# Performance work log

Measured on AMD Instinct MI355X. Metric: run time of the kernel, lower is better.

## Reference

```python
import jax, jax.numpy as jnp
import numpy as np

DIM = 384
HEADS = 6
HEAD_DIM = 64
WIN = 14
SCALE = HEAD_DIM ** -0.5
EPS = 1e-5  # torch LayerNorm default


def setup_inputs() -> dict:
    key = jax.random.key(0)
    ks = jax.random.split(key, 8)
    w = lambda k, shape: jax.random.normal(k, shape, dtype=jnp.float32) * 0.02
    return {
        "x": jax.random.normal(ks[0], (1, 336, 336, DIM), dtype=jnp.float32),
        "qkv_w": w(ks[1], (DIM, 3 * DIM)),
        "qkv_b": jnp.zeros((3 * DIM,), jnp.float32),
        "proj_w": w(ks[2], (DIM, DIM)),
        "proj_b": jnp.zeros((DIM,), jnp.float32),
        "rel_pos_h": w(ks[3], (2 * WIN - 1, HEAD_DIM)),
        "rel_pos_w": w(ks[4], (2 * WIN - 1, HEAD_DIM)),
        "norm1_w": jnp.ones((DIM,), jnp.float32),
        "norm1_b": jnp.zeros((DIM,), jnp.float32),
        "norm2_w": jnp.ones((DIM,), jnp.float32),
        "norm2_b": jnp.zeros((DIM,), jnp.float32),
        "fc1_w": w(ks[5], (DIM, 4 * DIM)),
        "fc1_b": jnp.zeros((4 * DIM,), jnp.float32),
        "fc2_w": w(ks[6], (4 * DIM, DIM)),
        "fc2_b": jnp.zeros((DIM,), jnp.float32),
    }


def _layernorm(x, w, b):
    m = jnp.mean(x, axis=-1, keepdims=True)
    v = jnp.var(x, axis=-1, keepdims=True)
    return (x - m) / jnp.sqrt(v + EPS) * w + b


def _rel_table(rel_pos):
    coords = np.arange(WIN)[:, None] - np.arange(WIN)[None, :] + (WIN - 1)
    return rel_pos[coords]


def _block(x, qkv_w, qkv_b, proj_w, proj_b, rel_pos_h, rel_pos_w,
           norm1_w, norm1_b, norm2_w, norm2_b, fc1_w, fc1_b, fc2_w, fc2_b):
    B, H, W, C = x.shape
    shortcut = x
    x = _layernorm(x, norm1_w, norm1_b)

    nH, nW = H // WIN, W // WIN
    xw = x.reshape(B, nH, WIN, nW, WIN, C).transpose(0, 1, 3, 2, 4, 5)
    xw = xw.reshape(B * nH * nW, WIN * WIN, C)  # [Nw, 196, C]
    Nw, L = xw.shape[0], WIN * WIN

    # --- attention with decomposed rel-pos ---
    qkv = xw @ qkv_w + qkv_b                         # [Nw, 196, 3C]
    qkv = qkv.reshape(Nw, L, 3, HEADS, HEAD_DIM).transpose(2, 0, 3, 1, 4)
    q, k, v = qkv[0], qkv[1], qkv[2]                 # [Nw, h, 196, d]

    attn = jnp.einsum("bhqd,bhkd->bhqk", q * SCALE, k)  # [Nw, h, 196, 196]

    Rh = _rel_table(rel_pos_h)                       # [14, 14, d]
    Rw = _rel_table(rel_pos_w)
    r_q = q.reshape(Nw, HEADS, WIN, WIN, HEAD_DIM)
    rel_h = jnp.einsum("bnhwc,hkc->bnhwk", r_q, Rh)  # [Nw, h, 14, 14, 14]
    rel_w = jnp.einsum("bnhwc,wkc->bnhwk", r_q, Rw)
    attn = (attn.reshape(Nw, HEADS, WIN, WIN, WIN, WIN)
            + rel_h[..., :, None] + rel_w[..., None, :]).reshape(Nw, HEADS, L, L)

    attn = jax.nn.softmax(attn, axis=-1)
    out = jnp.einsum("bhqk,bhkd->bhqd", attn, v)     # [Nw, h, 196, d]
    out = out.transpose(0, 2, 1, 3).reshape(Nw, L, C)
    out = out @ proj_w + proj_b

    # --- window unpartition ---
    out = out.reshape(B, nH, nW, WIN, WIN, C).transpose(0, 1, 3, 2, 4, 5)
    out = out.reshape(B, H, W, C)

    x = shortcut + out
    h = _layernorm(x, norm2_w, norm2_b)
    h = jax.nn.gelu(h @ fc1_w + fc1_b, approximate=False) @ fc2_w + fc2_b
    return x + h


def reference(x, qkv_w, qkv_b, proj_w, proj_b, rel_pos_h, rel_pos_w,
              norm1_w, norm1_b, norm2_w, norm2_b, fc1_w, fc1_b, fc2_w, fc2_b):
    return _block(x, qkv_w, qkv_b, proj_w, proj_b, rel_pos_h, rel_pos_w,
                  norm1_w, norm1_b, norm2_w, norm2_b, fc1_w, fc1_b, fc2_w, fc2_b)
```

## Files before the change

kernel.cpp:

```cpp
#include <hip/hip_runtime.h>
#include <math.h>

#define TOKENS 112896
#define C      384
#define NQKV   1152
#define NFC    1536
#define HEADS  6
#define HD     64
#define WIN    14
#define L      196
#define NWS    24
#define SCALEF 0.125f

typedef unsigned int  u32;
typedef unsigned short u16;
typedef short short8 __attribute__((ext_vector_type(8)));
typedef float floatx4 __attribute__((ext_vector_type(4)));

__device__ __forceinline__ u16 f2bf(float f) {
  u32 u = __float_as_uint(f);
  u += 0x7FFFu + ((u >> 16) & 1u);
  return (u16)(u >> 16);
}

__device__ __forceinline__ float bf2f(u16 v) {
  return __uint_as_float((u32)v << 16);
}

__device__ __forceinline__ u32 pk2bf(float lo, float hi) {
  u32 r;
  asm("v_cvt_pk_bf16_f32 %0, %1, %2" : "=v"(r) : "v"(lo), "v"(hi));
  return r;
}

__device__ __forceinline__ float gelu_f(float v) {
  float z = fabsf(v) * 0.70710678118654752f;
  float t = 1.0f / (1.0f + 0.3275911f * z);
  float poly = t * (0.254829592f + t * (-0.284496736f + t * (1.421413741f +
               t * (-1.453152027f + t * 1.061405429f))));
  float erfv = 1.0f - poly * __expf(-z * z);
  erfv = copysignf(erfv, v);
  return 0.5f * v * (1.0f + erfv);
}

__device__ __forceinline__ void async16(u16* lds, const u16* g) {
  __builtin_amdgcn_global_load_lds((const __attribute__((address_space(1))) void*)g,
                                   (__attribute__((address_space(3))) void*)lds,
                                   16, 0, 0);
}

__device__ __forceinline__ int win_to_tok(int r) {
  int n = r / L, l = r % L;
  int wh = n / NWS, ww = n % NWS;
  int ih = l / WIN, iw = l % WIN;
  return (wh * WIN + ih) * 336 + ww * WIN + iw;
}

__global__ __launch_bounds__(256) void conv_t_kernel(const float* __restrict__ in,
    u16* __restrict__ out, int K, int N)
{
  __shared__ u16 tile[32][33];
  const int kb = blockIdx.y * 32, nb = blockIdx.x * 32;
  const int tx = threadIdx.x & 31, ty = threadIdx.x >> 5;
#pragma unroll
  for (int i = 0; i < 4; i++) {
    int k = kb + ty + i * 8;
    tile[ty + i * 8][tx] = f2bf(in[(size_t)k * N + nb + tx]);
  }
  __syncthreads();
#pragma unroll
  for (int i = 0; i < 4; i++) {
    int n = nb + ty + i * 8;
    out[(size_t)n * K + kb + tx] = tile[tx][ty + i * 8];
  }
}

template<bool PERMUTE>
__global__ __launch_bounds__(128) void ln_kernel(const float* __restrict__ x,
    const float* __restrict__ w, const float* __restrict__ b,
    u16* __restrict__ out)
{
  const int t = blockIdx.x;
  const int tid = threadIdx.x;
  const float* xr = x + (size_t)t * C;
  float v0 = xr[tid], v1 = xr[tid + 128], v2 = xr[tid + 256];
  float s  = v0 + v1 + v2;
  float ss = v0 * v0 + v1 * v1 + v2 * v2;
#pragma unroll
  for (int off = 32; off > 0; off >>= 1) {
    s  += __shfl_down(s, off);
    ss += __shfl_down(ss, off);
  }
  __shared__ float red[4];
  if ((tid & 63) == 0) { red[(tid >> 6) * 2 + 0] = s; red[(tid >> 6) * 2 + 1] = ss; }
  __syncthreads();
  float S  = red[0] + red[2];
  float SS = red[1] + red[3];
  float mean = S * (1.0f / C);
  float var  = SS * (1.0f / C) - mean * mean;
  float rstd = rsqrtf(var + 1e-5f);
  size_t orow;
  if (PERMUTE) {
    int h_ = t / 336, w_ = t % 336;
    int wh = h_ / WIN, ih = h_ % WIN;
    int ww = w_ / WIN, iw = w_ % WIN;
    orow = (size_t)((wh * NWS + ww) * L + ih * WIN + iw);
  } else {
    orow = (size_t)t;
  }
  u16* op = out + orow * C;
  op[tid]       = f2bf((v0 - mean) * rstd * w[tid]       + b[tid]);
  op[tid + 128] = f2bf((v1 - mean) * rstd * w[tid + 128] + b[tid + 128]);
  op[tid + 256] = f2bf((v2 - mean) * rstd * w[tid + 256] + b[tid + 256]);
}

template<int MODE>
__global__ __launch_bounds__(256, 4) void gemm_bf16(
    const u16* __restrict__ A, const u16* __restrict__ Bt,
    const float* __restrict__ bias, const float* __restrict__ res,
    void* __restrict__ outv, int N, int K)
{
  __shared__ u16 As[2][128 * 32];
  __shared__ u16 Bs[2][128 * 32];
  const int tid = threadIdx.x;
  const int w = tid >> 6, l = tid & 63;

  const int nwg = gridDim.x * gridDim.y;
  int lin = blockIdx.y * gridDim.x + blockIdx.x;
  {
    int q8 = nwg >> 3, r8 = nwg & 7;
    int xcd = lin & 7, sub = lin >> 3;
    lin = (xcd < r8 ? xcd * (q8 + 1) : r8 * (q8 + 1) + (xcd - r8) * q8) + sub;
  }
  const int bx = lin % gridDim.x, by = lin / gridDim.x;
  const int bm = by * 128, bn = bx * 128;

  const int wm = (w >> 1) * 64, wn = (w & 1) * 64;
  const int lm = l & 15, quad = l >> 4;

  floatx4 acc[4][4] = {};

  u32 aofs[2], bofs[2];
#pragma unroll
  for (int q = 0; q < 2; q++) {
    int t = q * 256 + tid;
    int r = t >> 2, gl = t & 3;
    int sg = gl ^ ((r >> 1) & 3);
    aofs[q] = (u32)((bm + r) * K + sg * 8);
    bofs[q] = (u32)((bn + r) * K + sg * 8);
  }
  u16* Ad[2]; u16* Bd[2];
#pragma unroll
  for (int q = 0; q < 2; q++) {
    Ad[q] = &As[0][(q * 256 + w * 64) * 8];
    Bd[q] = &Bs[0][(q * 256 + w * 64) * 8];
  }

#define STAGE(buf, kt)                                         \
  {                                                            \
    const u16* Ap = A  + (kt);                                 \
    const u16* Bp = Bt + (kt);                                 \
    _Pragma("unroll")                                          \
    for (int q = 0; q < 2; q++) {                              \
      async16(Ad[q] + (buf) * 4096, Ap + aofs[q]);             \
      async16(Bd[q] + (buf) * 4096, Bp + bofs[q]);             \
    }                                                          \
  }

  const int xg = (quad ^ ((lm >> 1) & 3)) * 8;
  const u16* ard[4]; const u16* brd[4];
#pragma unroll
  for (int i = 0; i < 4; i++) {
    ard[i] = &As[0][(wm + i * 16 + lm) * 32 + xg];
    brd[i] = &Bs[0][(wn + i * 16 + lm) * 32 + xg];
  }

#define COMPUTE(BO)                                                         \
  {                                                                         \
    short8 bfr[4];                                                          \
    _Pragma("unroll")                                                       \
    for (int i2 = 0; i2 < 4; i2++)                                          \
      bfr[i2] = *(const short8*)(brd[i2] + (BO));                           \
    _Pragma("unroll")                                                       \
    for (int j2 = 0; j2 < 4; j2++) {                                        \
      short8 afr = *(const short8*)(ard[j2] + (BO));                        \
      _Pragma("unroll")                                                     \
      for (int i2 = 0; i2 < 4; i2++)                                        \
        acc[i2][j2] = __builtin_amdgcn_mfma_f32_16x16x32_bf16(              \
            bfr[i2], afr, acc[i2][j2], 0, 0, 0);                            \
    }                                                                       \
  }

  const int nk = K >> 5;
  STAGE(0, 0);
  __syncthreads();

  for (int t = 0; t < nk; t += 2) {
    STAGE(1, (t + 1) << 5);
    COMPUTE(0);
    __syncthreads();
    if (t + 2 < nk) STAGE(0, (t + 2) << 5);
    COMPUTE(4096);
    __syncthreads();
  }
#undef STAGE
#undef COMPUTE

  float4 bb[4];
#pragma unroll
  for (int i = 0; i < 4; i++)
    bb[i] = *(const float4*)&bias[bn + wn + i * 16 + quad * 4];

#pragma unroll
  for (int j = 0; j < 4; j++) {
    int m = bm + wm + j * 16 + lm;
    size_t ro;
    if (MODE == 1) ro = (size_t)win_to_tok(m) * N;
    else           ro = (size_t)m * N;
#pragma unroll
    for (int i = 0; i < 4; i++) {
      int n0 = bn + wn + i * 16 + quad * 4;
      float v0 = acc[i][j][0] + bb[i].x;
      float v1 = acc[i][j][1] + bb[i].y;
      float v2 = acc[i][j][2] + bb[i].z;
      float v3 = acc[i][j][3] + bb[i].w;
      if (MODE == 0) {
        uint2 st = make_uint2(pk2bf(v0, v1), pk2bf(v2, v3));
        *(uint2*)((u16*)outv + ro + n0) = st;
      } else if (MODE == 2) {
        uint2 st = make_uint2(pk2bf(gelu_f(v0), gelu_f(v1)),
                              pk2bf(gelu_f(v2), gelu_f(v3)));
        *(uint2*)((u16*)outv + ro + n0) = st;
      } else {
        float4 r4 = *(const float4*)&res[ro + n0];
        float4 o = make_float4(v0 + r4.x, v1 + r4.y, v2 + r4.z, v3 + r4.w);
        *(float4*)&((float*)outv)[ro + n0] = o;
      }
    }
  }
}

__global__ __launch_bounds__(256, 2) void attn_kernel(
    const u16* __restrict__ qkv,
    const float* __restrict__ relh, const float* __restrict__ relw,
    u16* __restrict__ out)
{
  __shared__ float Plds[4][512];
  __shared__ u16 rhlds[208 * 28];
  __shared__ u16 rwlds[208 * 28];
  __shared__ u16 Klds[32 * 64];
  __shared__ u16 Vtl[64 * 40];

  const int n = blockIdx.x / HEADS;
  const int h = blockIdx.x % HEADS;
  const int tid = threadIdx.x;
  const int w = tid >> 6;
  const int l = tid & 63;
  const int lm = l & 15;
  const int quad = l >> 4;
  const size_t base = (size_t)n * L;

  short8 qf[4][2];
#pragma unroll
  for (int i = 0; i < 4; i++) {
    int rt = w + 4 * i;
    if (rt <= 12) {
      int row = rt * 16 + lm; if (row > 195) row = 195;
      const u16* qp = qkv + (base + row) * NQKV + h * HD + quad * 8;
#pragma unroll
      for (int kf = 0; kf < 2; kf++)
        qf[i][kf] = *(const short8*)(qp + kf * 32);
    }
  }

  {
    short8 tf[2][2][2];
#pragma unroll
    for (int tab = 0; tab < 2; tab++) {
      const float* tp = tab ? relw : relh;
#pragma unroll
      for (int ct = 0; ct < 2; ct++) {
        int t = ct * 16 + lm;
#pragma unroll
        for (int kf = 0; kf < 2; kf++) {
          short8 v = {0, 0, 0, 0, 0, 0, 0, 0};
          if (t < 27) {
            const float* p = tp + t * HD + kf * 32 + quad * 8;
            float4 a = *(const float4*)p;
            float4 b = *(const float4*)(p + 4);
            v[0] = (short)f2bf(a.x); v[1] = (short)f2bf(a.y);
            v[2] = (short)f2bf(a.z); v[3] = (short)f2bf(a.w);
            v[4] = (short)f2bf(b.x); v[5] = (short)f2bf(b.y);
            v[6] = (short)f2bf(b.z); v[7] = (short)f2bf(b.w);
          }
          tf[tab][ct][kf] = v;
        }
      }
    }
#pragma unroll
    for (int i = 0; i < 4; i++) {
      int rt = w + 4 * i;
      if (rt > 12) continue;
#pragma unroll
      for (int tab = 0; tab < 2; tab++) {
        u16* dst = tab ? rwlds : rhlds;
#pragma unroll
        for (int ct = 0; ct < 2; ct++) {
          floatx4 acc = {};
          acc = __builtin_amdgcn_mfma_f32_16x16x32_bf16(qf[i][0], tf[tab][ct][0], acc, 0, 0, 0);
          acc = __builtin_amdgcn_mfma_f32_16x16x32_bf16(qf[i][1], tf[tab][ct][1], acc, 0, 0, 0);
          int t = ct * 16 + lm;
          if (t < 28) {
#pragma unroll
            for (int reg = 0; reg < 4; reg++) {
              int q = rt * 16 + quad * 4 + reg;
              dst[q * 28 + t] = f2bf(acc[reg]);
            }
          }
        }
      }
    }
  }

  floatx4 oacc[4][4] = {};
  float lsum[4][4] = {};

#pragma unroll 1
  for (int ks = 0; ks < 7; ks++) {
    __syncthreads();
    {
      int r = tid >> 3, g = tid & 7;
      int row = ks * 32 + r; if (row > 195) row = 195;
      uint4 kd = *(const uint4*)(qkv + (base + row) * NQKV + C + h * HD + g * 8);
      *(uint4*)&Klds[r * 64 + ((g ^ (r & 7)) * 8)] = kd;
    }
    {
      int r = tid & 31, seg = tid >> 5;
      int row = ks * 32 + r; if (row > 195) row = 195;
      uint4 vd = *(const uint4*)(qkv + (base + row) * NQKV + 2 * C + h * HD + seg * 8);
      union { uint4 u; u16 s[8]; } vv; vv.u = vd;
#pragma unroll
      for (int j = 0; j < 8; j++) Vtl[(seg * 8 + j) * 40 + r] = vv.s[j];
    }
    __syncthreads();

    short8 kfr[2][2];
#pragma unroll
    for (int ct = 0; ct < 2; ct++) {
      int krow = ct * 16 + lm;
#pragma unroll
      for (int kf = 0; kf < 2; kf++)
        kfr[ct][kf] = *(const short8*)&Klds[krow * 64 + (((kf * 4 + quad) ^ (krow & 7)) * 8)];
    }
    short8 vfr[4];
#pragma unroll
    for (int dt = 0; dt < 4; dt++)
      vfr[dt] = *(const short8*)&Vtl[(dt * 16 + lm) * 40 + quad * 8];

#pragma unroll
    for (int i = 0; i < 4; i++) {
      int rt = w + 4 * i;
      if (rt > 12) continue;
      floatx4 sc[2] = {};
#pragma unroll
      for (int ct = 0; ct < 2; ct++) {
        sc[ct] = __builtin_amdgcn_mfma_f32_16x16x32_bf16(qf[i][0], kfr[ct][0], sc[ct], 0, 0, 0);
        sc[ct] = __builtin_amdgcn_mfma_f32_16x16x32_bf16(qf[i][1], kfr[ct][1], sc[ct], 0, 0, 0);
      }
      float* Pw = Plds[w];
#pragma unroll
      for (int ct = 0; ct < 2; ct++) {
        int k = ks * 32 + ct * 16 + lm;
        int kh = (k * 293) >> 12;
        int kw2 = k - kh * 14;
        bool kval = (k < 196);
#pragma unroll
        for (int reg = 0; reg < 4; reg++) {
          int q = rt * 16 + quad * 4 + reg;
          int qh = (q * 293) >> 12;
          int qw = q - qh * 14;
          int th = qh - kh + 13; th = th < 0 ? 0 : th;
          int tw = qw - kw2 + 13;
          float bh = bf2f(rhlds[q * 28 + th]);
          float bw = bf2f(rwlds[q * 28 + tw]);
          float s = sc[ct][reg] * SCALEF + bh + bw;
          float p = kval ? __expf(s) : 0.0f;
          lsum[i][reg] += p;
          int prow = quad * 4 + reg;
          int col = ct * 16 + lm;
          Pw[prow * 32 + (((col >> 2) ^ (prow & 7)) * 4) + (col & 3)] = p;
        }
      }
      floatx4 pa = *(const floatx4*)&Pw[lm * 32 + (((2 * quad) ^ (lm & 7)) * 4)];
      floatx4 pb = *(const floatx4*)&Pw[lm * 32 + (((2 * quad + 1) ^ (lm & 7)) * 4)];
      short8 pfr;
#pragma unroll
      for (int j = 0; j < 4; j++) {
        pfr[j]     = (short)f2bf(pa[j]);
        pfr[4 + j] = (short)f2bf(pb[j]);
      }
#pragma unroll
      for (int dt = 0; dt < 4; dt++)
        oacc[i][dt] = __builtin_amdgcn_mfma_f32_16x16x32_bf16(pfr, vfr[dt], oacc[i][dt], 0, 0, 0);
    }
  }

#pragma unroll
  for (int i = 0; i < 4; i++) {
    int rt = w + 4 * i;
    if (rt > 12) continue;
#pragma unroll
    for (int reg = 0; reg < 4; reg++) {
      float v = lsum[i][reg];
      v += __shfl_xor(v, 1);
      v += __shfl_xor(v, 2);
      v += __shfl_xor(v, 4);
      v += __shfl_xor(v, 8);
      float inv = 1.0f / v;
      int row = rt * 16 + quad * 4 + reg;
      if (row < 196) {
        u16* op = out + (base + row) * C + h * HD + lm;
#pragma unroll
        for (int dt = 0; dt < 4; dt++) op[dt * 16] = f2bf(oacc[i][dt][reg] * inv);
      }
    }
  }
}

extern "C" void kernel_launch(void* const* d_in, const int* in_sizes, int n_in,
                              void* d_out, int out_size, void* d_ws, size_t ws_size,
                              hipStream_t stream)
{
  const float* x      = (const float*)d_in[0];
  const float* qkv_w  = (const float*)d_in[1];
  const float* qkv_b  = (const float*)d_in[2];
  const float* proj_w = (const float*)d_in[3];
  const float* proj_b = (const float*)d_in[4];
  const float* rel_h  = (const float*)d_in[5];
  const float* rel_w  = (const float*)d_in[6];
  const float* n1w    = (const float*)d_in[7];
  const float* n1b    = (const float*)d_in[8];
  const float* n2w    = (const float*)d_in[9];
  const float* n2b    = (const float*)d_in[10];
  const float* fc1_w  = (const float*)d_in[11];
  const float* fc1_b  = (const float*)d_in[12];
  const float* fc2_w  = (const float*)d_in[13];
  const float* fc2_b  = (const float*)d_in[14];

  u16*  W0 = (u16*)d_ws;
  u16*  W1 = (u16*)((char*)d_ws + 86704128);
  float* W2 = (float*)((char*)d_ws + 86704128 + 346816512);
  u16*  WT = (u16*)((char*)d_ws + 86704128 + 346816512 + 173408256);
  u16* qkv_wT  = WT;
  u16* proj_wT = qkv_wT + 442368;
  u16* fc1_wT  = proj_wT + 147456;
  u16* fc2_wT  = fc1_wT + 589824;

  conv_t_kernel<<<dim3(NQKV / 32, C / 32), 256, 0, stream>>>(qkv_w, qkv_wT, C, NQKV);
  conv_t_kernel<<<dim3(C / 32, C / 32), 256, 0, stream>>>(proj_w, proj_wT, C, C);
  conv_t_kernel<<<dim3(NFC / 32, C / 32), 256, 0, stream>>>(fc1_w, fc1_wT, C, NFC);
  conv_t_kernel<<<dim3(C / 32, NFC / 32), 256, 0, stream>>>(fc2_w, fc2_wT, NFC, C);

  ln_kernel<true><<<TOKENS, 128, 0, stream>>>(x, n1w, n1b, W0);
  gemm_bf16<0><<<dim3(NQKV / 128, TOKENS / 128), 256, 0, stream>>>(
      W0, qkv_wT, qkv_b, nullptr, W1, NQKV, C);
  attn_kernel<<<576 * HEADS, 256, 0, stream>>>(W1, rel_h, rel_w, W0);
  gemm_bf16<1><<<dim3(C / 128, TOKENS / 128), 256, 0, stream>>>(
      W0, proj_wT, proj_b, x, W2, C, C);
  ln_kernel<false><<<TOKENS, 128, 0, stream>>>(W2, n2w, n2b, W0);
  gemm_bf16<2><<<dim3(NFC / 128, TOKENS / 128), 256, 0, stream>>>(
      W0, fc1_wT, fc1_b, nullptr, W1, NFC, C);
  gemm_bf16<3><<<dim3(C / 128, TOKENS / 128), 256, 0, stream>>>(
      W1, fc2_wT, fc2_b, W2, (float*)d_out, C, NFC);
}
```

Measured before the change: 1.415 ms.

## Load GEMM MFMA fragments directly from global memory into registers, dropping LDS staging

Replaces the LDS double-buffered async global-to-LDS staging in the bf16 GEMM with direct per-lane global loads of MFMA fragments into registers, double-buffered in registers. This removes the LDS traffic and the __syncthreads barriers. In exchange, warps no longer share tiles, so global/L2 traffic for A and B rises. Register pressure also rises, so launch bounds occupancy drops from 4 to 3.

New measurement: 2.250 ms. 58.9% more time.

```diff
diff --git a/kernel.cpp b/kernel.cpp
--- a/kernel.cpp
+++ b/kernel.cpp
@@ -41,12 +41,6 @@
   float erfv = 1.0f - poly * __expf(-z * z);
   erfv = copysignf(erfv, v);
   return 0.5f * v * (1.0f + erfv);
-}
-
-__device__ __forceinline__ void async16(u16* lds, const u16* g) {
-  __builtin_amdgcn_global_load_lds((const __attribute__((address_space(1))) void*)g,
-                                   (__attribute__((address_space(3))) void*)lds,
-                                   16, 0, 0);
 }
 
 __device__ __forceinline__ int win_to_tok(int r) {
@@ -115,13 +109,11 @@
 }
 
 template<int MODE>
-__global__ __launch_bounds__(256, 4) void gemm_bf16(
+__global__ __launch_bounds__(256, 3) void gemm_bf16(
     const u16* __restrict__ A, const u16* __restrict__ Bt,
     const float* __restrict__ bias, const float* __restrict__ res,
     void* __restrict__ outv, int N, int K)
 {
-  __shared__ u16 As[2][128 * 32];
-  __shared__ u16 Bs[2][128 * 32];
   const int tid = threadIdx.x;
   const int w = tid >> 6, l = tid & 63;
 
@@ -140,71 +132,41 @@
 
   floatx4 acc[4][4] = {};
 
-  u32 aofs[2], bofs[2];
-#pragma unroll
-  for (int q = 0; q < 2; q++) {
-    int t = q * 256 + tid;
-    int r = t >> 2, gl = t & 3;
-    int sg = gl ^ ((r >> 1) & 3);
-    aofs[q] = (u32)((bm + r) * K + sg * 8);
-    bofs[q] = (u32)((bn + r) * K + sg * 8);
-  }
-  u16* Ad[2]; u16* Bd[2];
-#pragma unroll
-  for (int q = 0; q < 2; q++) {
-    Ad[q] = &As[0][(q * 256 + w * 64) * 8];
-    Bd[q] = &Bs[0][(q * 256 + w * 64) * 8];
-  }
-
-#define STAGE(buf, kt)                                         \
-  {                                                            \
-    const u16* Ap = A  + (kt);                                 \
-    const u16* Bp = Bt + (kt);                                 \
-    _Pragma("unroll")                                          \
-    for (int q = 0; q < 2; q++) {                              \
-      async16(Ad[q] + (buf) * 4096, Ap + aofs[q]);             \
-      async16(Bd[q] + (buf) * 4096, Bp + bofs[q]);             \
-    }                                                          \
-  }
-
-  const int xg = (quad ^ ((lm >> 1) & 3)) * 8;
-  const u16* ard[4]; const u16* brd[4];
+  const u16* Ab[4]; const u16* Bb[4];
 #pragma unroll
   for (int i = 0; i < 4; i++) {
-    ard[i] = &As[0][(wm + i * 16 + lm) * 32 + xg];
-    brd[i] = &Bs[0][(wn + i * 16 + lm) * 32 + xg];
-  }
-
-#define COMPUTE(BO)                                                         \
-  {                                                                         \
-    short8 bfr[4];                                                          \
-    _Pragma("unroll")                                                       \
-    for (int i2 = 0; i2 < 4; i2++)                                          \
-      bfr[i2] = *(const short8*)(brd[i2] + (BO));                           \
-    _Pragma("unroll")                                                       \
-    for (int j2 = 0; j2 < 4; j2++) {                                        \
-      short8 afr = *(const short8*)(ard[j2] + (BO));                        \
-      _Pragma("unroll")                                                     \
-      for (int i2 = 0; i2 < 4; i2++)                                        \
-        acc[i2][j2] = __builtin_amdgcn_mfma_f32_16x16x32_bf16(              \
-            bfr[i2], afr, acc[i2][j2], 0, 0, 0);                            \
-    }                                                                       \
-  }
+    Ab[i] = A  + (size_t)(bm + wm + i * 16 + lm) * K + quad * 8;
+    Bb[i] = Bt + (size_t)(bn + wn + i * 16 + lm) * K + quad * 8;
+  }
+
+  short8 af0[4], bf0[4], af1[4], bf1[4];
+
+#define LDF(AF, BF, KT)                                   \
+  { _Pragma("unroll")                                     \
+    for (int i2 = 0; i2 < 4; i2++) {                      \
+      AF[i2] = *(const short8*)(Ab[i2] + (KT));           \
+      BF[i2] = *(const short8*)(Bb[i2] + (KT));           \
+    } }
+
+#define MM(AF, BF)                                                       \
+  { _Pragma("unroll")                                                    \
+    for (int j2 = 0; j2 < 4; j2++) {                                     \
+      _Pragma("unroll")                                                  \
+      for (int i2 = 0; i2 < 4; i2++)                                     \
+        acc[i2][j2] = __builtin_amdgcn_mfma_f32_16x16x32_bf16(           \
+            BF[i2], AF[j2], acc[i2][j2], 0, 0, 0);                       \
+    } }
 
   const int nk = K >> 5;
-  STAGE(0, 0);
-  __syncthreads();
-
+  LDF(af0, bf0, 0);
   for (int t = 0; t < nk; t += 2) {
-    STAGE(1, (t + 1) << 5);
-    COMPUTE(0);
-    __syncthreads();
-    if (t + 2 < nk) STAGE(0, (t + 2) << 5);
-    COMPUTE(4096);
-    __syncthreads();
-  }
-#undef STAGE
-#undef COMPUTE
+    LDF(af1, bf1, (t + 1) << 5);
+    MM(af0, bf0);
+    if (t + 2 < nk) LDF(af0, bf0, (t + 2) << 5);
+    MM(af1, bf1);
+  }
+#undef LDF
+#undef MM
 
   float4 bb[4];
 #pragma unroll
```
